# Optimization experiments

Hardware: AMD Instinct MI355X
Metric: run time of the kernel (lower is better)

Reference implementation:

```python
import jax, jax.numpy as jnp
import numpy as np

KERNEL = 3
STRIDE = 1
PAD = 1


def setup_inputs() -> dict:
    key = jax.random.key(0)
    k1, k2 = jax.random.split(key)
    x = jax.random.normal(k1, (16, 32, 512, 512), dtype=jnp.float32)
    # original init: torch.rand(O, I, k, k) / (k*k)
    kernels = jax.random.uniform(k2, (32, 32, KERNEL, KERNEL), dtype=jnp.float32) / (KERNEL * KERNEL)
    return {"x": x, "kernels": kernels}


def reference(x, kernels):
    # Equivalent math to the unfold+einsum im2col conv2d: pad, extract kxk
    # windows with stride, contract over (in_channels, kh, kw).
    # Expressed as a direct convolution (cross-correlation), which is the
    # same computation without materializing the 6D window tensor.
    out = jax.lax.conv_general_dilated(
        x, kernels,
        window_strides=(STRIDE, STRIDE),
        padding=((PAD, PAD), (PAD, PAD)),
        dimension_numbers=("NCHW", "OIHW", "NCHW"),
    )
    return out  # [B, out_channels, H_out, W_out]
```

## Files before the change

kernel.cpp:

```cpp
#include <hip/hip_runtime.h>
#include <hip/hip_bf16.h>

typedef __attribute__((ext_vector_type(8))) short bf16x8;
typedef __attribute__((ext_vector_type(4))) float f32x4;
typedef __attribute__((ext_vector_type(4))) unsigned int u32x4;

#define HW (512 * 512)
#define TW 64
#define SLOTS 6
#define PXG (SLOTS * 66)
#define TILE_B (4 * PXG * 16)
#define STAGE_HALF 19456
#define SREAL 18432
#define DUMMY (TILE_B + 2 * STAGE_HALF)

#define SCHED() __builtin_amdgcn_sched_barrier(0)

__device__ __forceinline__ unsigned short f2bf(float f) {
    unsigned u = __builtin_bit_cast(unsigned, f);
    u += 0x7FFFu + ((u >> 16) & 1u);
    return (unsigned short)(u >> 16);
}

__device__ __forceinline__ void gll16(const float* g, char* l) {
    __builtin_amdgcn_global_load_lds(
        (const __attribute__((address_space(1))) void*)g,
        (__attribute__((address_space(3))) void*)l, 16, 0, 0);
}

__device__ __forceinline__ void issue_stage(const float* __restrict__ xb, int row0,
                                            int w0, char* smem, int half, int wvu) {
    const int lane = (int)threadIdx.x & 63;
    char* base = smem + TILE_B + half * STAGE_HALF;
    #pragma unroll
    for (int i = 0; i < 5; ++i) {
        if (wvu == 3 && i == 4) continue;
        int ob = (wvu * 5 + i) * 1024;
        int o  = ob + lane * 16;
        int o2 = o < (SREAL - 1) ? o : (SREAL - 1);
        int ch = o2 / 576;
        int rem = o2 - ch * 576;
        int hh = rem / 288;
        int wl = (rem - hh * 288) >> 2;
        int row = row0 + hh; row = row < 511 ? row : 511;
        int cb = w0 - 4 + wl;
        cb = cb < 0 ? 0 : (cb > 508 ? 508 : cb);
        gll16(xb + (size_t)ch * HW + row * 512 + cb, base + ob);
    }
}

template<bool TRANS, bool GLL, bool BAR>
__device__ __forceinline__ void body(char* smem, const float* __restrict__ xb,
                                     float* __restrict__ ob, bf16x8 (&wf)[9][2],
                                     int srb, int half, int rowbase, int w0,
                                     int wv, int wvu, int col16, int g4) {
    if (GLL) issue_stage(xb, rowbase + 5, w0, smem, half ^ 1, wvu);

    if (TRANS) {
        const char* sb = smem + TILE_B + half * STAGE_HALF;
        const int rowA = rowbase + 3;
        #pragma unroll
        for (int k = 0; k < 3; ++k) {
            if (k == 2 && threadIdx.x >= 32) continue;
            int u = (k < 2) ? (int)threadIdx.x + k * 256 : 512 + (int)threadIdx.x;
            int g = u / 136, r = u - g * 136, sl = r / 68, ww = r - sl * 68;
            float v[8];
            int ba = g * 8 * 576 + sl * 288 + (ww + 3) * 4;
            #pragma unroll
            for (int j = 0; j < 8; ++j) v[j] = *(const float*)(sb + ba + j * 576);
            bool ok = (ww < 66) & ((unsigned)(w0 + ww - 1) < 512u) & (rowA + sl < 512);
            #pragma unroll
            for (int j = 0; j < 8; ++j) v[j] = ok ? v[j] : 0.f;
            unsigned q0 = (unsigned)f2bf(v[0]) | ((unsigned)f2bf(v[1]) << 16);
            unsigned q1 = (unsigned)f2bf(v[2]) | ((unsigned)f2bf(v[3]) << 16);
            unsigned q2 = (unsigned)f2bf(v[4]) | ((unsigned)f2bf(v[5]) << 16);
            unsigned q3 = (unsigned)f2bf(v[6]) | ((unsigned)f2bf(v[7]) << 16);
            int slot = srb + 4 + sl; if (slot >= SLOTS) slot -= SLOTS;
            int byte = (ww < 66) ? (g * PXG + slot * 66 + ww) * 16
                                 : (DUMMY + ((int)threadIdx.x & 63) * 16);
            u32x4 q = { q0, q1, q2, q3 };
            *(u32x4*)(smem + byte) = q;
        }
    }

    f32x4 acc[2][2];
    {
        f32x4 z = {0.f, 0.f, 0.f, 0.f};
        acc[0][0] = z; acc[0][1] = z; acc[1][0] = z; acc[1][1] = z;
    }
    int rs[3];
    #pragma unroll
    for (int dh = 0; dh < 3; ++dh) {
        int s = srb + (wv & 1) + dh; if (s >= SLOTS) s -= SLOTS;
        rs[dh] = s * 66;
    }
    const int wcb = (wv >> 1) * 32;
    const char* xg = smem + g4 * (PXG * 16);
    #pragma unroll
    for (int dh = 0; dh < 3; ++dh) {
        #pragma unroll
        for (int dw = 0; dw < 3; ++dw) {
            const int tap = dh * 3 + dw;
            #pragma unroll
            for (int m = 0; m < 2; ++m) {
                bf16x8 a = *(const bf16x8*)(xg + (rs[dh] + wcb + m * 16 + col16 + dw) * 16);
                acc[m][0] = __builtin_amdgcn_mfma_f32_16x16x32_bf16(a, wf[tap][0], acc[m][0], 0, 0, 0);
                acc[m][1] = __builtin_amdgcn_mfma_f32_16x16x32_bf16(a, wf[tap][1], acc[m][1], 0, 0, 0);
            }
        }
    }
    {
        float* orow = ob + (size_t)(rowbase + (wv & 1)) * 512 + w0 + wcb;
        #pragma unroll
        for (int m = 0; m < 2; ++m)
            #pragma unroll
            for (int n = 0; n < 2; ++n)
                *(f32x4*)(orow + (size_t)(n * 16 + col16) * HW + m * 16 + g4 * 4) = acc[m][n];
    }

    if (BAR) {
        asm volatile("s_waitcnt vmcnt(4)" ::: "memory");
        SCHED();
        asm volatile("s_waitcnt lgkmcnt(0)" ::: "memory");
        SCHED();
        __builtin_amdgcn_s_barrier();
        SCHED();
    }
}

__global__ __launch_bounds__(256, 2)
void conv3x3_mfma(const float* __restrict__ x,
                  const float* __restrict__ wk,
                  float* __restrict__ out) {
    __shared__ __align__(16) char smem[DUMMY + 1024];

    const int tid   = (int)threadIdx.x;
    const int lane  = tid & 63;
    const int wv    = tid >> 6;
    const int wvu   = __builtin_amdgcn_readfirstlane(wv);
    const int col16 = lane & 15;
    const int g4    = lane >> 4;

    const int wg  = (int)blockIdx.x;
    const int xcd = wg & 7;
    const int i   = wg >> 3;
    const int xq  = i & 7;
    const int pg  = xcd + 8 * (i >> 3);
    const int yq  = pg & 7;
    const int zq  = pg >> 3;

    const int w0    = xq * TW;
    const int hbase = yq * 64;
    const int b     = zq;

    const float* xb = x + (size_t)b * 32 * HW;
    float* ob = out + (size_t)b * 32 * HW;

    {
        float* ws = (float*)(smem + TILE_B);
        for (int i2 = tid; i2 < 9216; i2 += 256) {
            int oc = i2 / 288;
            ws[oc * 289 + (i2 - oc * 288)] = wk[i2];
        }
    }
    float svp[5][8];
    #pragma unroll
    for (int k = 0; k < 5; ++k) {
        if (k == 4 && tid >= 32) continue;
        int u = (k < 4) ? tid + k * 256 : 1024 + tid;
        int g = u / 264, p = u - g * 264, hh = p / 66, ww = p - hh * 66;
        int row = hbase + hh - 1, cl = w0 + ww - 1;
        bool ok = ((unsigned)row < 512u) & ((unsigned)cl < 512u);
        int rowc = row < 0 ? 0 : (row > 511 ? 511 : row);
        int clc  = cl  < 0 ? 0 : (cl  > 511 ? 511 : cl);
        const float* src = xb + (size_t)(g * 8) * HW + rowc * 512 + clc;
        #pragma unroll
        for (int j = 0; j < 8; ++j) { float v = src[(size_t)j * HW]; svp[k][j] = ok ? v : 0.f; }
    }
    __syncthreads();

    bf16x8 wf[9][2];
    {
        const float* ws = (const float*)(smem + TILE_B);
        #pragma unroll
        for (int tap = 0; tap < 9; ++tap) {
            #pragma unroll
            for (int n = 0; n < 2; ++n) {
                bf16x8 f;
                #pragma unroll
                for (int j = 0; j < 8; ++j)
                    f[j] = (short)f2bf(ws[(n * 16 + col16) * 289 + (g4 * 8 + j) * 9 + tap]);
                wf[tap][n] = f;
            }
        }
    }
    __syncthreads();

    #pragma unroll
    for (int k = 0; k < 5; ++k) {
        if (k == 4 && tid >= 32) continue;
        int u = (k < 4) ? tid + k * 256 : 1024 + tid;
        int g = u / 264, p = u - g * 264;
        unsigned q0 = (unsigned)f2bf(svp[k][0]) | ((unsigned)f2bf(svp[k][1]) << 16);
        unsigned q1 = (unsigned)f2bf(svp[k][2]) | ((unsigned)f2bf(svp[k][3]) << 16);
        unsigned q2 = (unsigned)f2bf(svp[k][4]) | ((unsigned)f2bf(svp[k][5]) << 16);
        unsigned q3 = (unsigned)f2bf(svp[k][6]) | ((unsigned)f2bf(svp[k][7]) << 16);
        u32x4 q = { q0, q1, q2, q3 };
        *(u32x4*)(smem + (g * PXG + p) * 16) = q;
    }
    issue_stage(xb, hbase + 3, w0, smem, 0, wvu);
    __syncthreads();

    int srb = 0;
    #pragma unroll 1
    for (int t = 0; t < 30; ++t) {
        body<1, 1, 1>(smem, xb, ob, wf, srb, t & 1, hbase + 2 * t, w0, wv, wvu, col16, g4);
        srb += 2; if (srb >= SLOTS) srb -= SLOTS;
    }
    body<1, 0, 1>(smem, xb, ob, wf, srb, 0, hbase + 60, w0, wv, wvu, col16, g4);
    srb += 2; if (srb >= SLOTS) srb -= SLOTS;
    body<0, 0, 0>(smem, xb, ob, wf, srb, 1, hbase + 62, w0, wv, wvu, col16, g4);
}

extern "C" void kernel_launch(void* const* d_in, const int* in_sizes, int n_in,
                              void* d_out, int out_size, void* d_ws, size_t ws_size,
                              hipStream_t stream) {
    const float* x  = (const float*)d_in[0];
    const float* wk = (const float*)d_in[1];
    float* out = (float*)d_out;
    conv3x3_mfma<<<dim3(1024, 1, 1), 256, 0, stream>>>(x, wk, out);
}
```

Measured before the change: 249.0 us.

## Triple-buffer async global-to-LDS staging with two-stage prefetch distance

Result: no change. 250.7 us (+0.7%).

```diff
diff --git a/kernel.cpp b/kernel.cpp
--- a/kernel.cpp
+++ b/kernel.cpp
@@ -10,9 +10,8 @@
 #define SLOTS 6
 #define PXG (SLOTS * 66)
 #define TILE_B (4 * PXG * 16)
-#define STAGE_HALF 19456
-#define SREAL 18432
-#define DUMMY (TILE_B + 2 * STAGE_HALF)
+#define STAGE_SZ 18432
+#define DUMMY (TILE_B + 3 * STAGE_SZ)
 
 #define SCHED() __builtin_amdgcn_sched_barrier(0)
 
@@ -29,17 +28,16 @@
 }
 
 __device__ __forceinline__ void issue_stage(const float* __restrict__ xb, int row0,
-                                            int w0, char* smem, int half, int wvu) {
+                                            int w0, char* smem, int sidx, int wvu) {
     const int lane = (int)threadIdx.x & 63;
-    char* base = smem + TILE_B + half * STAGE_HALF;
+    char* base = smem + TILE_B + sidx * STAGE_SZ;
     #pragma unroll
     for (int i = 0; i < 5; ++i) {
-        if (wvu == 3 && i == 4) continue;
-        int ob = (wvu * 5 + i) * 1024;
+        int j = wvu * 5 + i;
+        int ob = (j < 18 ? j : 17) * 1024;
         int o  = ob + lane * 16;
-        int o2 = o < (SREAL - 1) ? o : (SREAL - 1);
-        int ch = o2 / 576;
-        int rem = o2 - ch * 576;
+        int ch = o / 576;
+        int rem = o - ch * 576;
         int hh = rem / 288;
         int wl = (rem - hh * 288) >> 2;
         int row = row0 + hh; row = row < 511 ? row : 511;
@@ -49,15 +47,15 @@
     }
 }
 
-template<bool TRANS, bool GLL, bool BAR>
+template<int W, bool TRANS, bool GLL, bool BAR>
 __device__ __forceinline__ void body(char* smem, const float* __restrict__ xb,
                                      float* __restrict__ ob, bf16x8 (&wf)[9][2],
-                                     int srb, int half, int rowbase, int w0,
+                                     int srb, int sc, int si, int rowbase, int w0,
                                      int wv, int wvu, int col16, int g4) {
-    if (GLL) issue_stage(xb, rowbase + 5, w0, smem, half ^ 1, wvu);
+    if (GLL) issue_stage(xb, rowbase + 7, w0, smem, si, wvu);
 
     if (TRANS) {
-        const char* sb = smem + TILE_B + half * STAGE_HALF;
+        const char* sb = smem + TILE_B + sc * STAGE_SZ;
         const int rowA = rowbase + 3;
         #pragma unroll
         for (int k = 0; k < 3; ++k) {
@@ -119,7 +117,8 @@
     }
 
     if (BAR) {
-        asm volatile("s_waitcnt vmcnt(4)" ::: "memory");
+        if constexpr (W == 9) asm volatile("s_waitcnt vmcnt(9)" ::: "memory");
+        else                  asm volatile("s_waitcnt vmcnt(4)" ::: "memory");
         SCHED();
         asm volatile("s_waitcnt lgkmcnt(0)" ::: "memory");
         SCHED();
@@ -208,18 +207,30 @@
         u32x4 q = { q0, q1, q2, q3 };
         *(u32x4*)(smem + (g * PXG + p) * 16) = q;
     }
+    SCHED();
     issue_stage(xb, hbase + 3, w0, smem, 0, wvu);
-    __syncthreads();
+    issue_stage(xb, hbase + 5, w0, smem, 1, wvu);
+    SCHED();
+    asm volatile("s_waitcnt vmcnt(5)" ::: "memory");
+    SCHED();
+    asm volatile("s_waitcnt lgkmcnt(0)" ::: "memory");
+    SCHED();
+    __builtin_amdgcn_s_barrier();
+    SCHED();
 
     int srb = 0;
     #pragma unroll 1
-    for (int t = 0; t < 30; ++t) {
-        body<1, 1, 1>(smem, xb, ob, wf, srb, t & 1, hbase + 2 * t, w0, wv, wvu, col16, g4);
+    for (int t = 0; t < 29; ++t) {
+        int sc = t % 3;
+        int si = sc + 2; if (si >= 3) si -= 3;
+        body<9, 1, 1, 1>(smem, xb, ob, wf, srb, sc, si, hbase + 2 * t, w0, wv, wvu, col16, g4);
         srb += 2; if (srb >= SLOTS) srb -= SLOTS;
     }
-    body<1, 0, 1>(smem, xb, ob, wf, srb, 0, hbase + 60, w0, wv, wvu, col16, g4);
+    body<4, 1, 0, 1>(smem, xb, ob, wf, srb, 2, 0, hbase + 58, w0, wv, wvu, col16, g4);
     srb += 2; if (srb >= SLOTS) srb -= SLOTS;
-    body<0, 0, 0>(smem, xb, ob, wf, srb, 1, hbase + 62, w0, wv, wvu, col16, g4);
+    body<4, 1, 0, 1>(smem, xb, ob, wf, srb, 0, 0, hbase + 60, w0, wv, wvu, col16, g4);
+    srb += 2; if (srb >= SLOTS) srb -= SLOTS;
+    body<4, 0, 0, 0>(smem, xb, ob, wf, srb, 0, 0, hbase + 62, w0, wv, wvu, col16, g4);
 }
 
 extern "C" void kernel_launch(void* const* d_in, const int* in_sizes, int n_in,
```
